# Kernel optimization log

Hardware: AMD Instinct MI355X
Metric: run time of the kernel (lower is better)

## Reference

```python
import jax, jax.numpy as jnp
import numpy as np

B, V, N, C = 32, 5, 196, 768
H = 768          # hidden_dim of score MLP
NUM_ITERS = 3


def setup_inputs() -> dict:
    key = jax.random.key(0)
    ks = jax.random.split(key, 6)
    scale = 1.0 / np.sqrt(C)
    x = jax.random.normal(ks[0], (B, V, N, C), dtype=jnp.float32)
    # per-view projection weights, stacked: [V, C, C] (no bias)
    w_views = jax.random.uniform(ks[1], (V, C, C), dtype=jnp.float32, minval=-scale, maxval=scale)
    # score MLP: Linear(2C -> H), Tanh, Linear(H -> 1)
    s1 = 1.0 / np.sqrt(2 * C)
    w1 = jax.random.uniform(ks[2], (2 * C, H), dtype=jnp.float32, minval=-s1, maxval=s1)
    b1 = jax.random.uniform(ks[3], (H,), dtype=jnp.float32, minval=-s1, maxval=s1)
    s2 = 1.0 / np.sqrt(H)
    w2 = jax.random.uniform(ks[4], (H, 1), dtype=jnp.float32, minval=-s2, maxval=s2)
    b2 = jax.random.uniform(ks[5], (1,), dtype=jnp.float32, minval=-s2, maxval=s2)
    return {"x": x, "w_views": w_views, "w1": w1, "b1": b1, "w2": w2, "b2": b2}


def reference(x, w_views, w1, b1, w2, b2):
    # x: [B, V, N, C]
    c = x.mean(axis=1)                                   # [B, N, C]
    # per-view projections are independent of c: compute once (same math)
    proj_x = jnp.einsum('bvnc,vcd->bvnd', x, w_views)    # [B, V, N, C]
    a = None
    for _ in range(NUM_ITERS):
        c_exp = jnp.broadcast_to(c[:, None], x.shape)    # [B, V, N, C]
        si = jnp.concatenate([x, c_exp], axis=-1)        # [B, V, N, 2C]
        h = jnp.tanh(jnp.einsum('bvnk,kh->bvnh', si, w1) + b1)
        s = (jnp.einsum('bvnh,ho->bvno', h, w2) + b2)[..., 0]  # [B, V, N]
        a = jax.nn.softmax(s, axis=1)                    # softmax over views
        c = jnp.einsum('bvn,bvnc->bnc', a, proj_x)       # weighted sum over V
    eps = 1e-8
    entropy = -(a * jnp.log(a + eps)).sum(axis=1)        # [B, N]
    r = 1.0 - entropy / np.log(V)
    return c, r
```

## Files before the change

### kernel.cpp

```cpp
#include <hip/hip_runtime.h>

#define CDIM   768
#define NSEQ   196
#define NVIEW  5
#define BN_TOT 6272
#define SLAB   4816896
#define WSLAB  589824

typedef __attribute__((ext_vector_type(8))) short short8;
typedef __attribute__((ext_vector_type(4))) float f32x4;

__device__ __forceinline__ float bf_lo(unsigned u) { return __uint_as_float(u << 16); }
__device__ __forceinline__ float bf_hi(unsigned u) { return __uint_as_float(u & 0xffff0000u); }
__device__ __forceinline__ unsigned short f2bf(float f) {
  unsigned u = __float_as_uint(f);
  return (unsigned short)((u + 0x7fffu + ((u >> 16) & 1u)) >> 16);
}
__device__ __forceinline__ unsigned pack2(float f0, float f1) {
  return (unsigned)f2bf(f0) | ((unsigned)f2bf(f1) << 16);
}
__device__ __forceinline__ float ftanh(float x) {
  x = fminf(fmaxf(x, -10.f), 10.f);
  float e = __expf(2.f * x);
  return (e - 1.f) / (e + 1.f);
}
__device__ __forceinline__ void async_cp16(const void* g, void* l) {
  __builtin_amdgcn_global_load_lds((const __attribute__((address_space(1))) unsigned*)g,
                                   (__attribute__((address_space(3))) unsigned*)l, 16, 0, 0);
}

__global__ __launch_bounds__(256) void k_tr(const float* __restrict__ wv,
                                            const float* __restrict__ w1,
                                            unsigned short* __restrict__ wvT,
                                            unsigned short* __restrict__ w1aT,
                                            unsigned short* __restrict__ w1bT) {
  __shared__ float tile[32][33];
  const int m = blockIdx.z;
  const float* src;
  unsigned short* dst;
  if (m < NVIEW)      { src = wv + (size_t)m * WSLAB; dst = wvT + (size_t)m * WSLAB; }
  else if (m == NVIEW){ src = w1;                     dst = w1aT; }
  else                { src = w1 + WSLAB;             dst = w1bT; }
  const int tx = threadIdx.x, ty = threadIdx.y;
  const int x0 = blockIdx.x * 32, y0 = blockIdx.y * 32;
#pragma unroll
  for (int i = 0; i < 4; ++i)
    tile[ty + i * 8][tx] = src[(size_t)(y0 + ty + i * 8) * CDIM + x0 + tx];
  __syncthreads();
#pragma unroll
  for (int i = 0; i < 4; ++i)
    dst[(size_t)(x0 + ty + i * 8) * CDIM + y0 + tx] = f2bf(tile[tx][ty + i * 8]);
}

__global__ __launch_bounds__(192) void k_cvt_mean(const float* __restrict__ x,
                                                  unsigned short* __restrict__ xb,
                                                  unsigned short* __restrict__ cb) {
  const int bn = blockIdx.x;
  const int b = bn / NSEQ, n = bn % NSEQ;
  const int h = threadIdx.x * 4;
  const float* xp = x + ((size_t)(b * NVIEW) * NSEQ + n) * CDIM + h;
  float s0 = 0, s1 = 0, s2 = 0, s3 = 0;
#pragma unroll
  for (int v = 0; v < NVIEW; ++v) {
    float4 p = *(const float4*)(xp + (size_t)v * (NSEQ * CDIM));
    s0 += p.x; s1 += p.y; s2 += p.z; s3 += p.w;
    uint2 q; q.x = pack2(p.x, p.y); q.y = pack2(p.z, p.w);
    *(uint2*)(xb + ((size_t)v * BN_TOT + bn) * CDIM + h) = q;
  }
  uint2 o;
  o.x = pack2(s0 * 0.2f, s1 * 0.2f);
  o.y = pack2(s2 * 0.2f, s3 * 0.2f);
  *(uint2*)(cb + (size_t)bn * CDIM + h) = o;
}

template <int MODE, int TOTAL, int CHUNK>
__global__ __launch_bounds__(256, 4) void gemm_bt(const unsigned short* __restrict__ P0,
                                                  const unsigned short* __restrict__ P1,
                                                  const unsigned short* __restrict__ P2,
                                                  const unsigned short* __restrict__ P3,
                                                  const unsigned short* __restrict__ P4,
                                                  unsigned short* __restrict__ Q0,
                                                  unsigned short* __restrict__ Q1,
                                                  unsigned short* __restrict__ Q2) {
  const int bid = blockIdx.x;
  const int work = (bid & 7) * CHUNK + (bid >> 3);
  if (work >= TOTAL) return;
  const int nt = work % 6;
  const int wq = work / 6;
  const int mt = wq % 49, z = wq / 49;

  __shared__ __align__(16) unsigned short ldsA[128 * 32];
  __shared__ __align__(16) unsigned short ldsB[128 * 32];
  const int t = threadIdx.x, w = t >> 6, lane = t & 63;
  const int lr = lane & 15, lq = lane >> 4;
  const int wm = (w >> 1) * 64, wn = (w & 1) * 64;
  const unsigned short *A, *Bt;
  unsigned short* C;
  if (MODE == 0) {
    if (z == 10) { A = P1; Bt = P4; C = Q2; }
    else if (z < 5)  { A = P0 + (size_t)z * SLAB;       Bt = P2 + (size_t)z * WSLAB; C = Q0 + (size_t)z * SLAB; }
    else             { A = P0 + (size_t)(z - 5) * SLAB; Bt = P3;                     C = Q1 + (size_t)(z - 5) * SLAB; }
  } else {
    A = P0 + (size_t)z * SLAB; Bt = P4; C = Q0 + (size_t)z * SLAB;
  }

  const unsigned short* ga0 = A + ((size_t)mt * 128 + (t >> 2)) * CDIM + (t & 3) * 8;
  const unsigned short* ga1 = ga0 + (size_t)64 * CDIM;
  const unsigned short* gb0 = Bt + ((size_t)nt * 128 + (t >> 2)) * CDIM + (t & 3) * 8;
  const unsigned short* gb1 = gb0 + (size_t)64 * CDIM;

  f32x4 acc[4][4] = {};
  for (int k0 = 0; k0 < CDIM; k0 += 32) {
    __syncthreads();
    async_cp16(ga0 + k0, &ldsA[w * 512]);
    async_cp16(ga1 + k0, &ldsA[2048 + w * 512]);
    async_cp16(gb0 + k0, &ldsB[w * 512]);
    async_cp16(gb1 + k0, &ldsB[2048 + w * 512]);
    __syncthreads();
    short8 af[4], bv[4];
#pragma unroll
    for (int i = 0; i < 4; ++i) af[i] = *(const short8*)&ldsA[(wm + i * 16 + lr) * 32 + lq * 8];
#pragma unroll
    for (int j = 0; j < 4; ++j) bv[j] = *(const short8*)&ldsB[(wn + j * 16 + lr) * 32 + lq * 8];
#pragma unroll
    for (int i = 0; i < 4; ++i)
#pragma unroll
      for (int j = 0; j < 4; ++j)
        acc[i][j] = __builtin_amdgcn_mfma_f32_16x16x32_bf16(af[i], bv[j], acc[i][j], 0, 0, 0);
  }
#pragma unroll
  for (int i = 0; i < 4; ++i)
#pragma unroll
    for (int j = 0; j < 4; ++j) {
      const int gc = nt * 128 + wn + j * 16 + lr;
      const int gr = mt * 128 + wm + i * 16 + lq * 4;
#pragma unroll
      for (int r = 0; r < 4; ++r)
        C[(size_t)(gr + r) * CDIM + gc] = f2bf(acc[i][j][r]);
    }
}

__global__ __launch_bounds__(192) void k_iter3(const unsigned short* __restrict__ xw1b,
                                               const unsigned short* __restrict__ cw1,
                                               const unsigned short* __restrict__ pw1b,
                                               const unsigned short* __restrict__ projb,
                                               const float* __restrict__ b1,
                                               const float* __restrict__ w2,
                                               float* __restrict__ outc,
                                               float* __restrict__ outr) {
  __shared__ float red[3][NVIEW];
  __shared__ float aa[NVIEW];
  const int bn = blockIdx.x, t = threadIdx.x, wid = t >> 6, lane = t & 63;
  const int h = t * 4;
  const float4 bv = *(const float4*)(b1 + h);
  const float4 wv = *(const float4*)(w2 + h);
  float cw[4];
  { uint2 c = *(const uint2*)(cw1 + (size_t)bn * CDIM + h);
    cw[0] = bf_lo(c.x); cw[1] = bf_hi(c.x); cw[2] = bf_lo(c.y); cw[3] = bf_hi(c.y); }
  float xw[NVIEW][4], pf[NVIEW][4];
#pragma unroll
  for (int v = 0; v < NVIEW; ++v) {
    uint2 q = *(const uint2*)(xw1b + ((size_t)v * BN_TOT + bn) * CDIM + h);
    xw[v][0] = bf_lo(q.x) + bv.x; xw[v][1] = bf_hi(q.x) + bv.y;
    xw[v][2] = bf_lo(q.y) + bv.z; xw[v][3] = bf_hi(q.y) + bv.w;
    uint2 p = *(const uint2*)(pw1b + ((size_t)v * BN_TOT + bn) * CDIM + h);
    pf[v][0] = bf_lo(p.x); pf[v][1] = bf_hi(p.x);
    pf[v][2] = bf_lo(p.y); pf[v][3] = bf_hi(p.y);
  }
  for (int it = 0; it < 3; ++it) {
    float part[NVIEW];
#pragma unroll
    for (int v = 0; v < NVIEW; ++v) {
      float p;
      p = wv.x * ftanh(xw[v][0] + cw[0]);
      p = fmaf(wv.y, ftanh(xw[v][1] + cw[1]), p);
      p = fmaf(wv.z, ftanh(xw[v][2] + cw[2]), p);
      p = fmaf(wv.w, ftanh(xw[v][3] + cw[3]), p);
      part[v] = p;
    }
#pragma unroll
    for (int off = 32; off > 0; off >>= 1)
#pragma unroll
      for (int v = 0; v < NVIEW; ++v) part[v] += __shfl_down(part[v], off);
    if (lane == 0)
#pragma unroll
      for (int v = 0; v < NVIEW; ++v) red[wid][v] = part[v];
    __syncthreads();
    if (t == 0) {
      float s[NVIEW];
#pragma unroll
      for (int v = 0; v < NVIEW; ++v) s[v] = red[0][v] + red[1][v] + red[2][v];
      float m = s[0];
#pragma unroll
      for (int v = 1; v < NVIEW; ++v) m = fmaxf(m, s[v]);
      float a[NVIEW], sum = 0.f;
#pragma unroll
      for (int v = 0; v < NVIEW; ++v) { a[v] = __expf(s[v] - m); sum += a[v]; }
      const float inv = 1.f / sum;
#pragma unroll
      for (int v = 0; v < NVIEW; ++v) { a[v] *= inv; aa[v] = a[v]; }
      if (it == 2) {
        float ent = 0.f;
#pragma unroll
        for (int v = 0; v < NVIEW; ++v) ent -= a[v] * logf(a[v] + 1e-8f);
        outr[bn] = 1.f - ent * 0.6213349345596119f;
      }
    }
    __syncthreads();
    if (it < 2) {
      float n0 = 0, n1 = 0, n2 = 0, n3 = 0;
#pragma unroll
      for (int v = 0; v < NVIEW; ++v) {
        const float av = aa[v];
        n0 = fmaf(av, pf[v][0], n0); n1 = fmaf(av, pf[v][1], n1);
        n2 = fmaf(av, pf[v][2], n2); n3 = fmaf(av, pf[v][3], n3);
      }
      cw[0] = n0; cw[1] = n1; cw[2] = n2; cw[3] = n3;
    } else {
      float r0 = 0, r1 = 0, r2 = 0, r3 = 0;
#pragma unroll
      for (int v = 0; v < NVIEW; ++v) {
        const float av = aa[v];
        uint2 p = *(const uint2*)(projb + ((size_t)v * BN_TOT + bn) * CDIM + h);
        r0 = fmaf(av, bf_lo(p.x), r0); r1 = fmaf(av, bf_hi(p.x), r1);
        r2 = fmaf(av, bf_lo(p.y), r2); r3 = fmaf(av, bf_hi(p.y), r3);
      }
      float4 of; of.x = r0; of.y = r1; of.z = r2; of.w = r3;
      *(float4*)(outc + (size_t)bn * CDIM + h) = of;
    }
  }
}

extern "C" void kernel_launch(void* const* d_in, const int* in_sizes, int n_in,
                              void* d_out, int out_size, void* d_ws, size_t ws_size,
                              hipStream_t stream) {
  (void)in_sizes; (void)n_in; (void)out_size; (void)ws_size;
  const float* x  = (const float*)d_in[0];
  const float* wv = (const float*)d_in[1];
  const float* w1 = (const float*)d_in[2];
  const float* b1 = (const float*)d_in[3];
  const float* w2 = (const float*)d_in[4];

  unsigned short* ws   = (unsigned short*)d_ws;
  unsigned short* wvT  = ws;
  unsigned short* w1aT = ws + 2949120;
  unsigned short* w1bT = ws + 3538944;
  unsigned short* xb   = ws + 4128768;
  unsigned short* pw1b = ws + 4128768;
  unsigned short* projb= ws + 28213248;
  unsigned short* xw1b = ws + 52297728;
  unsigned short* cb   = ws + 76382208;
  unsigned short* cw1  = ws + 81199104;

  float* outc = (float*)d_out;
  float* outr = outc + SLAB;

  k_tr<<<dim3(24, 24, 7), dim3(32, 8), 0, stream>>>(wv, w1, wvT, w1aT, w1bT);
  k_cvt_mean<<<BN_TOT, 192, 0, stream>>>(x, xb, cb);
  gemm_bt<0, 3234, 405><<<3240, 256, 0, stream>>>(xb, cb, wvT, w1aT, w1bT, projb, xw1b, cw1);
  gemm_bt<1, 1470, 184><<<1472, 256, 0, stream>>>(projb, nullptr, nullptr, nullptr, w1bT,
                                                  pw1b, nullptr, nullptr);
  k_iter3<<<BN_TOT, 192, 0, stream>>>(xw1b, cw1, pw1b, projb, b1, w2, outc, outr);
}
```

Baseline: 375.1 us.

## Replace 128x128 GEMM with 256x256 multi-stage pipelined swizzled LDS kernel

Replaces the bf16 GEMM kernel with a 512-thread version that computes 256x256 output tiles. It uses a 4-buffer, 3-deep async global-to-LDS prefetch pipeline with XOR-swizzled LDS layout, split A/B staging interleaved with MFMA phases, s_setprio around the MFMA blocks, and XCD-aware remapping of block IDs. The goal is more data reuse per tile, hiding global-load latency behind MFMA work, and fewer LDS bank conflicts than the single-buffered, barrier-heavy loop it replaces. In exchange it uses 128KB of dynamic LDS and many accumulator registers, and the last M tile reads past 6272 rows. Only the stores are guarded against those extra rows.

```diff
diff --git a/kernel.cpp b/kernel.cpp
--- a/kernel.cpp
+++ b/kernel.cpp
@@ -73,8 +73,8 @@
   *(uint2*)(cb + (size_t)bn * CDIM + h) = o;
 }
 
-template <int MODE, int TOTAL, int CHUNK>
-__global__ __launch_bounds__(256, 4) void gemm_bt(const unsigned short* __restrict__ P0,
+template <int MODE>
+__global__ __launch_bounds__(512, 2) void gemm256(const unsigned short* __restrict__ P0,
                                                   const unsigned short* __restrict__ P1,
                                                   const unsigned short* __restrict__ P2,
                                                   const unsigned short* __restrict__ P3,
@@ -82,62 +82,104 @@
                                                   unsigned short* __restrict__ Q0,
                                                   unsigned short* __restrict__ Q1,
                                                   unsigned short* __restrict__ Q2) {
-  const int bid = blockIdx.x;
-  const int work = (bid & 7) * CHUNK + (bid >> 3);
-  if (work >= TOTAL) return;
-  const int nt = work % 6;
-  const int wq = work / 6;
-  const int mt = wq % 49, z = wq / 49;
-
-  __shared__ __align__(16) unsigned short ldsA[128 * 32];
-  __shared__ __align__(16) unsigned short ldsB[128 * 32];
-  const int t = threadIdx.x, w = t >> 6, lane = t & 63;
-  const int lr = lane & 15, lq = lane >> 4;
-  const int wm = (w >> 1) * 64, wn = (w & 1) * 64;
+  extern __shared__ unsigned short ldsb[];
+  constexpr int NWG = (MODE == 0) ? 825 : 375;
+  constexpr int NKT = CDIM / 32;
+  const int orig = blockIdx.x;
+  const int q = NWG >> 3, r = NWG & 7, xcd = orig & 7, slot = orig >> 3;
+  const int wgid = (xcd < r ? xcd * (q + 1) : r * (q + 1) + (xcd - r) * q) + slot;
+  const int nt = wgid % 3;
+  const int wq = wgid / 3;
+  const int mt = wq % 25, z = wq / 25;
+
   const unsigned short *A, *Bt;
   unsigned short* C;
   if (MODE == 0) {
-    if (z == 10) { A = P1; Bt = P4; C = Q2; }
-    else if (z < 5)  { A = P0 + (size_t)z * SLAB;       Bt = P2 + (size_t)z * WSLAB; C = Q0 + (size_t)z * SLAB; }
-    else             { A = P0 + (size_t)(z - 5) * SLAB; Bt = P3;                     C = Q1 + (size_t)(z - 5) * SLAB; }
+    if (z == 10)    { A = P1; Bt = P4; C = Q2; }
+    else if (z < 5) { A = P0 + (size_t)z * SLAB;       Bt = P2 + (size_t)z * WSLAB; C = Q0 + (size_t)z * SLAB; }
+    else            { A = P0 + (size_t)(z - 5) * SLAB; Bt = P3;                     C = Q1 + (size_t)(z - 5) * SLAB; }
   } else {
     A = P0 + (size_t)z * SLAB; Bt = P4; C = Q0 + (size_t)z * SLAB;
   }
 
-  const unsigned short* ga0 = A + ((size_t)mt * 128 + (t >> 2)) * CDIM + (t & 3) * 8;
-  const unsigned short* ga1 = ga0 + (size_t)64 * CDIM;
-  const unsigned short* gb0 = Bt + ((size_t)nt * 128 + (t >> 2)) * CDIM + (t & 3) * 8;
-  const unsigned short* gb1 = gb0 + (size_t)64 * CDIM;
-
-  f32x4 acc[4][4] = {};
-  for (int k0 = 0; k0 < CDIM; k0 += 32) {
-    __syncthreads();
-    async_cp16(ga0 + k0, &ldsA[w * 512]);
-    async_cp16(ga1 + k0, &ldsA[2048 + w * 512]);
-    async_cp16(gb0 + k0, &ldsB[w * 512]);
-    async_cp16(gb1 + k0, &ldsB[2048 + w * 512]);
-    __syncthreads();
-    short8 af[4], bv[4];
-#pragma unroll
-    for (int i = 0; i < 4; ++i) af[i] = *(const short8*)&ldsA[(wm + i * 16 + lr) * 32 + lq * 8];
-#pragma unroll
-    for (int j = 0; j < 4; ++j) bv[j] = *(const short8*)&ldsB[(wn + j * 16 + lr) * 32 + lq * 8];
+  const int t = threadIdx.x, w = t >> 6, lane = t & 63, lr = lane & 15, lq = lane >> 4;
+  const int wm = (w >> 2) << 7;
+  const int wn = (w & 3) << 6;
+
+  const int kc = (((t & 3) ^ ((t >> 3) & 3)) << 3);
+  const unsigned short* gA = A  + (size_t)(mt * 256 + (t >> 2)) * CDIM + kc;
+  const unsigned short* gB = Bt + (size_t)(nt * 256 + (t >> 2)) * CDIM + kc;
+
+  const int kch = ((lq ^ ((lr >> 1) & 3)) << 3);
+  const int raBase = (wm + lr) * 32 + kch;
+  const int rbBase = 8192 + (wn + lr) * 32 + kch;
+
+#define STAGE_A(st) { const unsigned short* s_ = gA + (st) * 32;                      \
+    unsigned short* d_ = ldsb + (((st) & 3) << 14) + (w << 9);                        \
+    async_cp16(s_, d_); async_cp16(s_ + (size_t)128 * CDIM, d_ + 4096); }
+#define STAGE_B(st) { const unsigned short* s_ = gB + (st) * 32;                      \
+    unsigned short* d_ = ldsb + (((st) & 3) << 14) + 8192 + (w << 9);                 \
+    async_cp16(s_, d_); async_cp16(s_ + (size_t)128 * CDIM, d_ + 4096); }
+
+  f32x4 acc[8][4] = {};
+
+  STAGE_A(0); STAGE_B(0);
+  STAGE_A(1); STAGE_B(1);
+  STAGE_A(2); STAGE_B(2);
+  asm volatile("s_waitcnt vmcnt(8)");
+  __builtin_amdgcn_s_barrier();
+
+  for (int kt = 0; kt < NKT; ++kt) {
+    const unsigned short* bufp = ldsb + ((kt & 3) << 14);
+    short8 af[4], bf[4];
+#pragma unroll
+    for (int j = 0; j < 4; ++j) bf[j] = *(const short8*)(bufp + rbBase + (j << 9));
+#pragma unroll
+    for (int i = 0; i < 4; ++i) af[i] = *(const short8*)(bufp + raBase + (i << 9));
+    if (kt + 3 < NKT) STAGE_A(kt + 3);
+    __builtin_amdgcn_s_barrier();
+    asm volatile("s_waitcnt lgkmcnt(0)");
+    __builtin_amdgcn_s_setprio(1);
 #pragma unroll
     for (int i = 0; i < 4; ++i)
 #pragma unroll
       for (int j = 0; j < 4; ++j)
-        acc[i][j] = __builtin_amdgcn_mfma_f32_16x16x32_bf16(af[i], bv[j], acc[i][j], 0, 0, 0);
-  }
-#pragma unroll
-  for (int i = 0; i < 4; ++i)
-#pragma unroll
-    for (int j = 0; j < 4; ++j) {
-      const int gc = nt * 128 + wn + j * 16 + lr;
-      const int gr = mt * 128 + wm + i * 16 + lq * 4;
-#pragma unroll
-      for (int r = 0; r < 4; ++r)
-        C[(size_t)(gr + r) * CDIM + gc] = f2bf(acc[i][j][r]);
-    }
+        acc[i][j] = __builtin_amdgcn_mfma_f32_16x16x32_bf16(af[i], bf[j], acc[i][j], 0, 0, 0);
+    __builtin_amdgcn_s_setprio(0);
+    __builtin_amdgcn_s_barrier();
+#pragma unroll
+    for (int i = 0; i < 4; ++i) af[i] = *(const short8*)(bufp + raBase + 2048 + (i << 9));
+    if (kt + 3 < NKT) STAGE_B(kt + 3);
+    __builtin_amdgcn_s_barrier();
+    asm volatile("s_waitcnt lgkmcnt(0)");
+    __builtin_amdgcn_s_setprio(1);
+#pragma unroll
+    for (int i = 0; i < 4; ++i)
+#pragma unroll
+      for (int j = 0; j < 4; ++j)
+        acc[4 + i][j] = __builtin_amdgcn_mfma_f32_16x16x32_bf16(af[i], bf[j], acc[4 + i][j], 0, 0, 0);
+    __builtin_amdgcn_s_setprio(0);
+    if (kt < NKT - 3)       { asm volatile("s_waitcnt vmcnt(8)"); }
+    else if (kt == NKT - 3) { asm volatile("s_waitcnt vmcnt(4)"); }
+    else if (kt == NKT - 2) { asm volatile("s_waitcnt vmcnt(0)"); }
+    __builtin_amdgcn_s_barrier();
+  }
+#undef STAGE_A
+#undef STAGE_B
+
+  if (mt * 256 + wm < BN_TOT) {
+    const size_t row0 = (size_t)(mt * 256 + wm + lq * 4);
+    const int col0 = nt * 256 + wn + lr;
+#pragma unroll
+    for (int fi = 0; fi < 8; ++fi)
+#pragma unroll
+      for (int j = 0; j < 4; ++j) {
+        unsigned short* cp = C + (row0 + fi * 16) * CDIM + col0 + j * 16;
+#pragma unroll
+        for (int rr = 0; rr < 4; ++rr)
+          cp[(size_t)rr * CDIM] = f2bf(acc[fi][j][rr]);
+      }
+  }
 }
 
 __global__ __launch_bounds__(192) void k_iter3(const unsigned short* __restrict__ xw1b,
@@ -257,8 +299,8 @@
 
   k_tr<<<dim3(24, 24, 7), dim3(32, 8), 0, stream>>>(wv, w1, wvT, w1aT, w1bT);
   k_cvt_mean<<<BN_TOT, 192, 0, stream>>>(x, xb, cb);
-  gemm_bt<0, 3234, 405><<<3240, 256, 0, stream>>>(xb, cb, wvT, w1aT, w1bT, projb, xw1b, cw1);
-  gemm_bt<1, 1470, 184><<<1472, 256, 0, stream>>>(projb, nullptr, nullptr, nullptr, w1bT,
-                                                  pw1b, nullptr, nullptr);
+  gemm256<0><<<825, 512, 131072, stream>>>(xb, cb, wvT, w1aT, w1bT, projb, xw1b, cw1);
+  gemm256<1><<<375, 512, 131072, stream>>>(projb, nullptr, nullptr, nullptr, w1bT,
+                                           pw1b, nullptr, nullptr);
   k_iter3<<<BN_TOT, 192, 0, stream>>>(xw1b, cw1, pw1b, projb, b1, w2, outc, outr);
 }
```

Result: no change. 376.3 us (+0.3%).

## Fold W1b into per-view weights and fuse x conversion into a pipelined GEMM

Applied to the files above, without the earlier changes.

Precomputes, per view, the product of the view projection weights with the second half of W1. This lets the proj·W1b term be computed straight from x in the same pass that produces proj and x·W1a, instead of in a dependent second GEMM over proj. The main GEMM now reads fp32 x directly and converts it to bf16 while staging into LDS, so the separate bf16 copy of x is no longer written or read. The GEMM moves to 512-thread blocks with 128x256 tiles, double-buffered swizzled LDS, setprio around the MFMAs and an XCD-aware work remap. The trade-off is a different bf16 rounding path through the pre-multiplied weights, plus more register and LDS pressure per block.

```diff
diff --git a/kernel.cpp b/kernel.cpp
--- a/kernel.cpp
+++ b/kernel.cpp
@@ -33,28 +33,33 @@
                                             const float* __restrict__ w1,
                                             unsigned short* __restrict__ wvT,
                                             unsigned short* __restrict__ w1aT,
-                                            unsigned short* __restrict__ w1bT) {
+                                            unsigned short* __restrict__ w1bT,
+                                            unsigned short* __restrict__ wvB) {
   __shared__ float tile[32][33];
   const int m = blockIdx.z;
   const float* src;
   unsigned short* dst;
-  if (m < NVIEW)      { src = wv + (size_t)m * WSLAB; dst = wvT + (size_t)m * WSLAB; }
+  unsigned short* dstB = nullptr;
+  if (m < NVIEW)      { src = wv + (size_t)m * WSLAB; dst = wvT + (size_t)m * WSLAB;
+                        dstB = wvB + (size_t)m * WSLAB; }
   else if (m == NVIEW){ src = w1;                     dst = w1aT; }
   else                { src = w1 + WSLAB;             dst = w1bT; }
   const int tx = threadIdx.x, ty = threadIdx.y;
   const int x0 = blockIdx.x * 32, y0 = blockIdx.y * 32;
 #pragma unroll
-  for (int i = 0; i < 4; ++i)
-    tile[ty + i * 8][tx] = src[(size_t)(y0 + ty + i * 8) * CDIM + x0 + tx];
+  for (int i = 0; i < 4; ++i) {
+    float v = src[(size_t)(y0 + ty + i * 8) * CDIM + x0 + tx];
+    tile[ty + i * 8][tx] = v;
+    if (dstB) dstB[(size_t)(y0 + ty + i * 8) * CDIM + x0 + tx] = f2bf(v);
+  }
   __syncthreads();
 #pragma unroll
   for (int i = 0; i < 4; ++i)
     dst[(size_t)(x0 + ty + i * 8) * CDIM + y0 + tx] = f2bf(tile[tx][ty + i * 8]);
 }
 
-__global__ __launch_bounds__(192) void k_cvt_mean(const float* __restrict__ x,
-                                                  unsigned short* __restrict__ xb,
-                                                  unsigned short* __restrict__ cb) {
+__global__ __launch_bounds__(192) void k_mean(const float* __restrict__ x,
+                                              unsigned short* __restrict__ cb) {
   const int bn = blockIdx.x;
   const int b = bn / NSEQ, n = bn % NSEQ;
   const int h = threadIdx.x * 4;
@@ -64,8 +69,6 @@
   for (int v = 0; v < NVIEW; ++v) {
     float4 p = *(const float4*)(xp + (size_t)v * (NSEQ * CDIM));
     s0 += p.x; s1 += p.y; s2 += p.z; s3 += p.w;
-    uint2 q; q.x = pack2(p.x, p.y); q.y = pack2(p.z, p.w);
-    *(uint2*)(xb + ((size_t)v * BN_TOT + bn) * CDIM + h) = q;
   }
   uint2 o;
   o.x = pack2(s0 * 0.2f, s1 * 0.2f);
@@ -73,70 +76,124 @@
   *(uint2*)(cb + (size_t)bn * CDIM + h) = o;
 }
 
-template <int MODE, int TOTAL, int CHUNK>
-__global__ __launch_bounds__(256, 4) void gemm_bt(const unsigned short* __restrict__ P0,
-                                                  const unsigned short* __restrict__ P1,
-                                                  const unsigned short* __restrict__ P2,
-                                                  const unsigned short* __restrict__ P3,
-                                                  const unsigned short* __restrict__ P4,
-                                                  unsigned short* __restrict__ Q0,
-                                                  unsigned short* __restrict__ Q1,
-                                                  unsigned short* __restrict__ Q2) {
-  const int bid = blockIdx.x;
-  const int work = (bid & 7) * CHUNK + (bid >> 3);
-  if (work >= TOTAL) return;
-  const int nt = work % 6;
-  const int wq = work / 6;
-  const int mt = wq % 49, z = wq / 49;
-
-  __shared__ __align__(16) unsigned short ldsA[128 * 32];
-  __shared__ __align__(16) unsigned short ldsB[128 * 32];
-  const int t = threadIdx.x, w = t >> 6, lane = t & 63;
-  const int lr = lane & 15, lq = lane >> 4;
-  const int wm = (w >> 1) * 64, wn = (w & 1) * 64;
-  const unsigned short *A, *Bt;
+template <int MODE>
+__global__ __launch_bounds__(512, 4) void gemm_f(const float* __restrict__ X,
+                                                 const unsigned short* __restrict__ P0,
+                                                 const unsigned short* __restrict__ P1,
+                                                 const unsigned short* __restrict__ P2,
+                                                 unsigned short* __restrict__ Q0,
+                                                 unsigned short* __restrict__ Q1,
+                                                 unsigned short* __restrict__ Q2) {
+  __shared__ __align__(16) unsigned short lds[2 * 12288];
+  constexpr int NWG = (MODE == 0) ? 2205 : (MODE == 1) ? 90 : 147;
+  constexpr int NKT = CDIM / 32;
+  const int orig = blockIdx.x;
+  const int qq = NWG >> 3, rr = NWG & 7, xcd = orig & 7, slot = orig >> 3;
+  const int wk = (xcd < rr ? xcd * (qq + 1) : rr * (qq + 1) + (xcd - rr) * qq) + slot;
+
+  const int t = threadIdx.x, w = t >> 6, lane = t & 63, lr = lane & 15, lq = lane >> 4;
+  const int wm = ((w >> 2) & 1) * 64;
+  const int wn = (w & 3) * 64;
+
+  const unsigned short* Abf = nullptr;
+  const unsigned short* Bt;
   unsigned short* C;
-  if (MODE == 0) {
-    if (z == 10) { A = P1; Bt = P4; C = Q2; }
-    else if (z < 5)  { A = P0 + (size_t)z * SLAB;       Bt = P2 + (size_t)z * WSLAB; C = Q0 + (size_t)z * SLAB; }
-    else             { A = P0 + (size_t)(z - 5) * SLAB; Bt = P3;                     C = Q1 + (size_t)(z - 5) * SLAB; }
+  const float* aPtr = nullptr;
+  int colBase, mrow0;
+  if constexpr (MODE == 0) {
+    const int v = wk / 441, rem = wk % 441;
+    const int mt = rem / 9, nt = rem % 9;
+    const int sub = nt / 3, ntl = nt % 3;
+    Bt = (sub == 0) ? P0 + (size_t)v * WSLAB : (sub == 1) ? P1 : P2 + (size_t)v * WSLAB;
+    C  = (sub == 0) ? Q0 + (size_t)v * SLAB  : (sub == 1) ? Q1 + (size_t)v * SLAB
+                                             : Q2 + (size_t)v * SLAB;
+    colBase = ntl * 256; mrow0 = mt * 128;
+    const int r = mrow0 + (t >> 2);
+    const int b = r / 196, n = r - b * 196;
+    aPtr = X + (size_t)((b * 5 + v) * 196 + n) * CDIM + (t & 3) * 8;
+  } else if constexpr (MODE == 1) {
+    const int v = wk / 18, rem = wk % 18;
+    const int mt = rem / 3, nt = rem % 3;
+    Abf = P0;
+    Bt  = P2 + (size_t)v * WSLAB;
+    C   = Q0 + (size_t)v * WSLAB;
+    colBase = nt * 256; mrow0 = mt * 128;
   } else {
-    A = P0 + (size_t)z * SLAB; Bt = P4; C = Q0 + (size_t)z * SLAB;
-  }
-
-  const unsigned short* ga0 = A + ((size_t)mt * 128 + (t >> 2)) * CDIM + (t & 3) * 8;
-  const unsigned short* ga1 = ga0 + (size_t)64 * CDIM;
-  const unsigned short* gb0 = Bt + ((size_t)nt * 128 + (t >> 2)) * CDIM + (t & 3) * 8;
-  const unsigned short* gb1 = gb0 + (size_t)64 * CDIM;
+    const int mt = wk / 3, nt = wk % 3;
+    Abf = P1;
+    Bt  = P0;
+    C   = Q0;
+    colBase = nt * 256; mrow0 = mt * 128;
+  }
+
+  const int swz = ((t & 3) ^ ((t >> 3) & 3)) << 3;
+  const unsigned short* gBp = Bt + (size_t)(colBase + (t >> 2)) * CDIM + swz;
+  const unsigned short* gAb = (MODE == 0) ? nullptr
+                            : Abf + (size_t)(mrow0 + (t >> 2)) * CDIM + swz;
+  const int aswz = swz;
+
+  const int kch = ((lq ^ ((lr >> 1) & 3)) << 3);
+
+#define STB(kt, s) { const unsigned short* sp_ = gBp + (kt) * 32;                 \
+    unsigned short* dp_ = lds + (s) * 12288 + 4096 + (w << 9);                    \
+    async_cp16(sp_, dp_); async_cp16(sp_ + (size_t)128 * CDIM, dp_ + 4096); }
+#define STA1(kt, s) { async_cp16(gAb + (kt) * 32, lds + (s) * 12288 + (w << 9)); }
+#define STA0W(s) { uint4 qv_;                                                     \
+    qv_.x = pack2(pa0.x, pa0.y); qv_.y = pack2(pa0.z, pa0.w);                     \
+    qv_.z = pack2(pa1.x, pa1.y); qv_.w = pack2(pa1.z, pa1.w);                     \
+    *(uint4*)(lds + (s) * 12288 + (t >> 2) * 32 + aswz) = qv_; }
 
   f32x4 acc[4][4] = {};
-  for (int k0 = 0; k0 < CDIM; k0 += 32) {
-    __syncthreads();
-    async_cp16(ga0 + k0, &ldsA[w * 512]);
-    async_cp16(ga1 + k0, &ldsA[2048 + w * 512]);
-    async_cp16(gb0 + k0, &ldsB[w * 512]);
-    async_cp16(gb1 + k0, &ldsB[2048 + w * 512]);
-    __syncthreads();
-    short8 af[4], bv[4];
-#pragma unroll
-    for (int i = 0; i < 4; ++i) af[i] = *(const short8*)&ldsA[(wm + i * 16 + lr) * 32 + lq * 8];
-#pragma unroll
-    for (int j = 0; j < 4; ++j) bv[j] = *(const short8*)&ldsB[(wn + j * 16 + lr) * 32 + lq * 8];
+  float4 pa0{}, pa1{};
+
+  if constexpr (MODE == 0) { pa0 = *(const float4*)(aPtr); pa1 = *(const float4*)(aPtr + 4); }
+  else                     { STA1(0, 0); }
+  STB(0, 0);
+  if constexpr (MODE == 0) STA0W(0);
+  asm volatile("s_waitcnt vmcnt(0) lgkmcnt(0)" ::: "memory");
+  __builtin_amdgcn_s_barrier();
+
+  for (int kt = 0; kt < NKT; ++kt) {
+    const int s = kt & 1;
+    const unsigned short* bp = lds + s * 12288;
+    const bool pf = (kt + 1 < NKT);
+    if (pf) {
+      if constexpr (MODE == 0) {
+        pa0 = *(const float4*)(aPtr + (kt + 1) * 32);
+        pa1 = *(const float4*)(aPtr + (kt + 1) * 32 + 4);
+      } else { STA1(kt + 1, s ^ 1); }
+      STB(kt + 1, s ^ 1);
+    }
+    short8 af[4], bf[4];
+#pragma unroll
+    for (int i = 0; i < 4; ++i) af[i] = *(const short8*)(bp + (wm + i * 16 + lr) * 32 + kch);
+#pragma unroll
+    for (int j = 0; j < 4; ++j) bf[j] = *(const short8*)(bp + 4096 + (wn + j * 16 + lr) * 32 + kch);
+    __builtin_amdgcn_s_setprio(1);
 #pragma unroll
     for (int i = 0; i < 4; ++i)
 #pragma unroll
       for (int j = 0; j < 4; ++j)
-        acc[i][j] = __builtin_amdgcn_mfma_f32_16x16x32_bf16(af[i], bv[j], acc[i][j], 0, 0, 0);
-  }
+        acc[i][j] = __builtin_amdgcn_mfma_f32_16x16x32_bf16(af[i], bf[j], acc[i][j], 0, 0, 0);
+    __builtin_amdgcn_s_setprio(0);
+    if (pf) { if constexpr (MODE == 0) STA0W(s ^ 1); }
+    asm volatile("s_waitcnt vmcnt(0) lgkmcnt(0)" ::: "memory");
+    __builtin_amdgcn_s_barrier();
+  }
+#undef STB
+#undef STA1
+#undef STA0W
+
 #pragma unroll
   for (int i = 0; i < 4; ++i)
 #pragma unroll
     for (int j = 0; j < 4; ++j) {
-      const int gc = nt * 128 + wn + j * 16 + lr;
-      const int gr = mt * 128 + wm + i * 16 + lq * 4;
+      const int gr = mrow0 + wm + i * 16 + lq * 4;
+      const int gc = colBase + wn + j * 16 + lr;
+      unsigned short* cp = C + (size_t)gr * CDIM + gc;
 #pragma unroll
       for (int r = 0; r < 4; ++r)
-        C[(size_t)(gr + r) * CDIM + gc] = f2bf(acc[i][j][r]);
+        cp[(size_t)r * CDIM] = f2bf(acc[i][j][r]);
     }
 }
 
@@ -245,20 +302,21 @@
   unsigned short* wvT  = ws;
   unsigned short* w1aT = ws + 2949120;
   unsigned short* w1bT = ws + 3538944;
-  unsigned short* xb   = ws + 4128768;
-  unsigned short* pw1b = ws + 4128768;
-  unsigned short* projb= ws + 28213248;
-  unsigned short* xw1b = ws + 52297728;
+  unsigned short* projb= ws + 4128768;
+  unsigned short* xw1b = ws + 28213248;
+  unsigned short* wvB  = ws + 28213248;
+  unsigned short* pw1b = ws + 52297728;
   unsigned short* cb   = ws + 76382208;
   unsigned short* cw1  = ws + 81199104;
+  unsigned short* wpT  = ws + 81199104;
 
   float* outc = (float*)d_out;
   float* outr = outc + SLAB;
 
-  k_tr<<<dim3(24, 24, 7), dim3(32, 8), 0, stream>>>(wv, w1, wvT, w1aT, w1bT);
-  k_cvt_mean<<<BN_TOT, 192, 0, stream>>>(x, xb, cb);
-  gemm_bt<0, 3234, 405><<<3240, 256, 0, stream>>>(xb, cb, wvT, w1aT, w1bT, projb, xw1b, cw1);
-  gemm_bt<1, 1470, 184><<<1472, 256, 0, stream>>>(projb, nullptr, nullptr, nullptr, w1bT,
-                                                  pw1b, nullptr, nullptr);
+  k_tr<<<dim3(24, 24, 7), dim3(32, 8), 0, stream>>>(wv, w1, wvT, w1aT, w1bT, wvB);
+  k_mean<<<BN_TOT, 192, 0, stream>>>(x, cb);
+  gemm_f<1><<<90, 512, 0, stream>>>(nullptr, w1bT, nullptr, wvB, wpT, nullptr, nullptr);
+  gemm_f<0><<<2205, 512, 0, stream>>>(x, wvT, w1aT, wpT, projb, xw1b, pw1b);
+  gemm_f<2><<<147, 512, 0, stream>>>(nullptr, w1bT, cb, nullptr, cw1, nullptr, nullptr);
   k_iter3<<<BN_TOT, 192, 0, stream>>>(xw1b, cw1, pw1b, projb, b1, w2, outc, outr);
 }
```

Result: slower. 401.4 us (+7.0%).

## Rewrite bf16 GEMM with 128x256 tiles, triple-buffered async LDS and swizzle

Applied to the files above, without the earlier changes.

Replaces the 128x128 single-buffered GEMM with a 512-thread kernel that computes 128x256 tiles. Global-to-LDS async copies now run through a three-stage ring, so loads for step k+2 overlap the MFMAs of step k, with one barrier per k-step instead of two. It also adds an XOR swizzle on the LDS k-chunks to reduce bank conflicts, raises wave priority around the MFMA block, and remaps block IDs so contiguous work lands on each XCD. In exchange it uses 72KB of dynamic LDS per block, which lowers occupancy, and the larger tiles give fewer workgroups.

```diff
diff --git a/kernel.cpp b/kernel.cpp
--- a/kernel.cpp
+++ b/kernel.cpp
@@ -73,70 +73,86 @@
   *(uint2*)(cb + (size_t)bn * CDIM + h) = o;
 }
 
-template <int MODE, int TOTAL, int CHUNK>
-__global__ __launch_bounds__(256, 4) void gemm_bt(const unsigned short* __restrict__ P0,
-                                                  const unsigned short* __restrict__ P1,
-                                                  const unsigned short* __restrict__ P2,
-                                                  const unsigned short* __restrict__ P3,
-                                                  const unsigned short* __restrict__ P4,
-                                                  unsigned short* __restrict__ Q0,
-                                                  unsigned short* __restrict__ Q1,
-                                                  unsigned short* __restrict__ Q2) {
-  const int bid = blockIdx.x;
-  const int work = (bid & 7) * CHUNK + (bid >> 3);
-  if (work >= TOTAL) return;
-  const int nt = work % 6;
-  const int wq = work / 6;
-  const int mt = wq % 49, z = wq / 49;
-
-  __shared__ __align__(16) unsigned short ldsA[128 * 32];
-  __shared__ __align__(16) unsigned short ldsB[128 * 32];
-  const int t = threadIdx.x, w = t >> 6, lane = t & 63;
-  const int lr = lane & 15, lq = lane >> 4;
-  const int wm = (w >> 1) * 64, wn = (w & 1) * 64;
+template <int MODE>
+__global__ __launch_bounds__(512, 4) void gemm_r(const unsigned short* __restrict__ P0,
+                                                 const unsigned short* __restrict__ cbp,
+                                                 const unsigned short* __restrict__ wvT,
+                                                 const unsigned short* __restrict__ w1aT,
+                                                 const unsigned short* __restrict__ w1bT,
+                                                 unsigned short* __restrict__ Q0,
+                                                 unsigned short* __restrict__ Q1,
+                                                 unsigned short* __restrict__ Q2) {
+  extern __shared__ unsigned short ldsb[];
+  constexpr int NWG = (MODE == 0) ? 1617 : 735;
+  const int orig = blockIdx.x;
+  const int qq = NWG >> 3, rr = NWG & 7, xcd = orig & 7, slot0 = orig >> 3;
+  const int wk = (xcd < rr ? xcd * (qq + 1) : rr * (qq + 1) + (xcd - rr) * qq) + slot0;
+  const int nt = wk % 3, mt = (wk / 3) % 49, z = wk / 147;
+
+  const int t = threadIdx.x, w = t >> 6, lane = t & 63, lr = lane & 15, lq = lane >> 4;
+  const int wm = ((w >> 2) & 1) * 64;
+  const int wn = (w & 3) * 64;
+  const int colBase = nt * 256, mrow0 = mt * 128;
+
   const unsigned short *A, *Bt;
   unsigned short* C;
   if (MODE == 0) {
-    if (z == 10) { A = P1; Bt = P4; C = Q2; }
-    else if (z < 5)  { A = P0 + (size_t)z * SLAB;       Bt = P2 + (size_t)z * WSLAB; C = Q0 + (size_t)z * SLAB; }
-    else             { A = P0 + (size_t)(z - 5) * SLAB; Bt = P3;                     C = Q1 + (size_t)(z - 5) * SLAB; }
+    if (z == 10)    { A = cbp; Bt = w1bT; C = Q2; }
+    else if (z < 5) { A = P0 + (size_t)z * SLAB;       Bt = wvT + (size_t)z * WSLAB; C = Q0 + (size_t)z * SLAB; }
+    else            { A = P0 + (size_t)(z - 5) * SLAB; Bt = w1aT;                    C = Q1 + (size_t)(z - 5) * SLAB; }
   } else {
-    A = P0 + (size_t)z * SLAB; Bt = P4; C = Q0 + (size_t)z * SLAB;
-  }
-
-  const unsigned short* ga0 = A + ((size_t)mt * 128 + (t >> 2)) * CDIM + (t & 3) * 8;
-  const unsigned short* ga1 = ga0 + (size_t)64 * CDIM;
-  const unsigned short* gb0 = Bt + ((size_t)nt * 128 + (t >> 2)) * CDIM + (t & 3) * 8;
-  const unsigned short* gb1 = gb0 + (size_t)64 * CDIM;
+    A = P0 + (size_t)z * SLAB; Bt = w1bT; C = Q0 + (size_t)z * SLAB;
+  }
+
+  const int swz = ((t & 3) ^ ((t >> 3) & 3)) << 3;
+  const unsigned short* gA = A  + (size_t)(mrow0 + (t >> 2)) * CDIM + swz;
+  const unsigned short* gB = Bt + (size_t)(colBase + (t >> 2)) * CDIM + swz;
+  const int kch = ((lq ^ ((lr >> 1) & 3)) << 3);
+
+#define STAGE(kt, s) {                                                            \
+    unsigned short* d_ = ldsb + (s) * 12288 + (w << 9);                           \
+    async_cp16(gA + (kt) * 32, d_);                                               \
+    async_cp16(gB + (kt) * 32, d_ + 4096);                                        \
+    async_cp16(gB + (kt) * 32 + (size_t)128 * CDIM, d_ + 8192); }
 
   f32x4 acc[4][4] = {};
-  for (int k0 = 0; k0 < CDIM; k0 += 32) {
-    __syncthreads();
-    async_cp16(ga0 + k0, &ldsA[w * 512]);
-    async_cp16(ga1 + k0, &ldsA[2048 + w * 512]);
-    async_cp16(gb0 + k0, &ldsB[w * 512]);
-    async_cp16(gb1 + k0, &ldsB[2048 + w * 512]);
-    __syncthreads();
-    short8 af[4], bv[4];
-#pragma unroll
-    for (int i = 0; i < 4; ++i) af[i] = *(const short8*)&ldsA[(wm + i * 16 + lr) * 32 + lq * 8];
-#pragma unroll
-    for (int j = 0; j < 4; ++j) bv[j] = *(const short8*)&ldsB[(wn + j * 16 + lr) * 32 + lq * 8];
+
+  STAGE(0, 0); STAGE(1, 1);
+  asm volatile("s_waitcnt vmcnt(3)" ::: "memory");
+  __builtin_amdgcn_s_barrier();
+
+  for (int kt = 0; kt < 24; ++kt) {
+    const int s = kt % 3;
+    const unsigned short* bp = ldsb + s * 12288;
+    if (kt < 22) STAGE(kt + 2, (kt + 2) % 3);
+    short8 af[4], bf[4];
+#pragma unroll
+    for (int i = 0; i < 4; ++i) af[i] = *(const short8*)(bp + (wm + i * 16 + lr) * 32 + kch);
+#pragma unroll
+    for (int j = 0; j < 4; ++j) bf[j] = *(const short8*)(bp + 4096 + (wn + j * 16 + lr) * 32 + kch);
+    __builtin_amdgcn_s_setprio(1);
 #pragma unroll
     for (int i = 0; i < 4; ++i)
 #pragma unroll
       for (int j = 0; j < 4; ++j)
-        acc[i][j] = __builtin_amdgcn_mfma_f32_16x16x32_bf16(af[i], bv[j], acc[i][j], 0, 0, 0);
-  }
+        acc[i][j] = __builtin_amdgcn_mfma_f32_16x16x32_bf16(af[i], bf[j], acc[i][j], 0, 0, 0);
+    __builtin_amdgcn_s_setprio(0);
+    if (kt < 22)       { asm volatile("s_waitcnt vmcnt(3)" ::: "memory"); }
+    else if (kt == 22) { asm volatile("s_waitcnt vmcnt(0)" ::: "memory"); }
+    __builtin_amdgcn_s_barrier();
+  }
+#undef STAGE
+
 #pragma unroll
   for (int i = 0; i < 4; ++i)
 #pragma unroll
     for (int j = 0; j < 4; ++j) {
-      const int gc = nt * 128 + wn + j * 16 + lr;
-      const int gr = mt * 128 + wm + i * 16 + lq * 4;
+      const int gr = mrow0 + wm + i * 16 + lq * 4;
+      const int gc = colBase + wn + j * 16 + lr;
+      unsigned short* cp = C + (size_t)gr * CDIM + gc;
 #pragma unroll
       for (int r = 0; r < 4; ++r)
-        C[(size_t)(gr + r) * CDIM + gc] = f2bf(acc[i][j][r]);
+        cp[(size_t)r * CDIM] = f2bf(acc[i][j][r]);
     }
 }
 
@@ -257,8 +273,8 @@
 
   k_tr<<<dim3(24, 24, 7), dim3(32, 8), 0, stream>>>(wv, w1, wvT, w1aT, w1bT);
   k_cvt_mean<<<BN_TOT, 192, 0, stream>>>(x, xb, cb);
-  gemm_bt<0, 3234, 405><<<3240, 256, 0, stream>>>(xb, cb, wvT, w1aT, w1bT, projb, xw1b, cw1);
-  gemm_bt<1, 1470, 184><<<1472, 256, 0, stream>>>(projb, nullptr, nullptr, nullptr, w1bT,
-                                                  pw1b, nullptr, nullptr);
+  gemm_r<0><<<1617, 512, 73728, stream>>>(xb, cb, wvT, w1aT, w1bT, projb, xw1b, cw1);
+  gemm_r<1><<<735, 512, 73728, stream>>>(projb, nullptr, nullptr, nullptr, w1bT,
+                                         pw1b, nullptr, nullptr);
   k_iter3<<<BN_TOT, 192, 0, stream>>>(xw1b, cw1, pw1b, projb, b1, w2, outc, outr);
 }
```

After: 357.2 us. -4.8%, faster.
